# Performance work log

Measured on AMD Instinct MI355X. Metric: run time of the kernel, lower is better.

The kernel has to match this reference:

```python
import jax, jax.numpy as jnp
import numpy as np

HEADS = 16
EMBED = 1024
HEAD_DIM = EMBED // HEADS

def _split_heads(x):
    b, n, _ = x.shape
    return x.reshape(b, n, HEADS, HEAD_DIM).transpose(0, 2, 1, 3)  # b h n d

def _merge_heads(x):
    b, h, n, d = x.shape
    return x.transpose(0, 2, 1, 3).reshape(b, n, h * d)

def _attn(q_in, kv_in, Wq, bq, Wk, bk, Wv, bv, Wo, bo):
    q = _split_heads(q_in @ Wq + bq)
    k = _split_heads(kv_in @ Wk + bk)
    v = _split_heads(kv_in @ Wv + bv)
    e = jnp.einsum('bhqd,bhkd->bhqk', q, k) * (HEAD_DIM ** -0.5)
    a = jax.nn.softmax(e, axis=-1)
    o = jnp.einsum('bhqk,bhkd->bhqd', a, v)
    return _merge_heads(o) @ Wo + bo

def _layernorm(x, g, b, eps=1e-5):
    mu = jnp.mean(x, axis=-1, keepdims=True)
    var = jnp.var(x, axis=-1, keepdims=True)
    return (x - mu) * jax.lax.rsqrt(var + eps) * g + b

def setup_inputs() -> dict:
    key = jax.random.key(0)
    ks = jax.random.split(key, 20)
    s = 0.02
    d = {
        'temp_features': jax.random.normal(ks[0], (2, 2048, EMBED), jnp.float32),
        'spat_features': jax.random.normal(ks[1], (2, 2048, EMBED), jnp.float32),
    }
    names = ['t2s_Wq', 't2s_Wk', 't2s_Wv', 't2s_Wo', 's2t_Wq', 's2t_Wk', 's2t_Wv', 's2t_Wo']
    for i, nm in enumerate(names):
        d[nm] = jax.random.normal(ks[2 + i], (EMBED, EMBED), jnp.float32) * s
        d[nm.replace('W', 'b')] = jnp.zeros((EMBED,), jnp.float32)
    d['ln_g'] = jnp.ones((EMBED,), jnp.float32)
    d['ln_b'] = jnp.zeros((EMBED,), jnp.float32)
    return d

def reference(temp_features, spat_features,
              t2s_Wq, t2s_bq, t2s_Wk, t2s_bk, t2s_Wv, t2s_bv, t2s_Wo, t2s_bo,
              s2t_Wq, s2t_bq, s2t_Wk, s2t_bk, s2t_Wv, s2t_bv, s2t_Wo, s2t_bo,
              ln_g, ln_b):
    # t2s: queries from spat, keys/values from temp; residual = spat
    t2s = _attn(spat_features, temp_features, t2s_Wq, t2s_bq, t2s_Wk, t2s_bk,
                t2s_Wv, t2s_bv, t2s_Wo, t2s_bo)
    t2s_out = _layernorm(spat_features + t2s, ln_g, ln_b)
    # s2t: queries from temp, keys/values from spat; residual = temp
    s2t = _attn(temp_features, spat_features, s2t_Wq, s2t_bq, s2t_Wk, s2t_bk,
                s2t_Wv, s2t_bv, s2t_Wo, s2t_bo)
    s2t_out = _layernorm(temp_features + s2t, ln_g, ln_b)
    return (s2t_out, t2s_out)
```

## Files before the change

kernel.cpp:

```cpp
#include <hip/hip_runtime.h>
#include <stdint.h>

#define SEQ 2048
#define EMB 1024
#define NROWS 4096

typedef __bf16 bf16x8 __attribute__((ext_vector_type(8)));
typedef float f32x4 __attribute__((ext_vector_type(4)));
typedef unsigned short ushort8 __attribute__((ext_vector_type(8)));

__device__ __forceinline__ unsigned short f2bf(float f) {
  unsigned int u = __float_as_uint(f);
  u += 0x7fffu + ((u >> 16) & 1u);
  return (unsigned short)(u >> 16);
}

__device__ __forceinline__ float bf2f(unsigned short h) {
  return __uint_as_float((unsigned int)h << 16);
}

__device__ __forceinline__ f32x4 mfma16(bf16x8 a, bf16x8 b, f32x4 c) {
  return __builtin_amdgcn_mfma_f32_16x16x32_bf16(a, b, c, 0, 0, 0);
}

__device__ __forceinline__ void async_load16(const void* g, void* l) {
  auto gp = reinterpret_cast<__attribute__((address_space(1))) void*>(
      reinterpret_cast<uintptr_t>(g));
  auto lp = reinterpret_cast<__attribute__((address_space(3))) void*>(
      reinterpret_cast<uintptr_t>(l));
  __builtin_amdgcn_global_load_lds(gp, lp, 16, 0, 0);
}

__global__ __launch_bounds__(256) void prep(const float* __restrict__ t,
                                            const float* __restrict__ s,
                                            unsigned short* __restrict__ tb,
                                            unsigned short* __restrict__ sb,
                                            const float* __restrict__ W0,
                                            const float* __restrict__ W1,
                                            const float* __restrict__ W2,
                                            const float* __restrict__ W3,
                                            const float* __restrict__ W4,
                                            const float* __restrict__ W5,
                                            const float* __restrict__ W6,
                                            const float* __restrict__ W7,
                                            unsigned short* __restrict__ Wt) {
  const int bx = blockIdx.x;
  if (bx < 8192) {
    int i = bx * 256 + threadIdx.x;
    const float* x; unsigned short* y;
    if (i < NROWS * EMB / 4) { x = t; y = tb; }
    else { x = s; y = sb; i -= NROWS * EMB / 4; }
    float4 v = ((const float4*)x)[i];
    ushort4 o;
    o.x = f2bf(v.x); o.y = f2bf(v.y); o.z = f2bf(v.z); o.w = f2bf(v.w);
    ((ushort4*)y)[i] = o;
    return;
  }
  const int e = bx - 8192;
  const int z = e >> 8, tt = e & 255;
  const float* Ws[8] = {W0, W1, W2, W3, W4, W5, W6, W7};
  const float* W = Ws[z];
  unsigned short* dst = Wt + ((size_t)z << 20);
  __shared__ unsigned short tile[64][65];
  const int n0 = (tt & 15) * 64, k0 = (tt >> 4) * 64;
#pragma unroll
  for (int i = 0; i < 16; ++i) {
    const int ee = i * 256 + threadIdx.x;
    const int kk = ee >> 6, nn = ee & 63;
    tile[kk][nn] = f2bf(W[(size_t)(k0 + kk) * EMB + n0 + nn]);
  }
  __syncthreads();
#pragma unroll
  for (int i = 0; i < 16; ++i) {
    const int ee = i * 256 + threadIdx.x;
    const int nn = ee >> 6, kk = ee & 63;
    dst[(size_t)(n0 + nn) * EMB + k0 + kk] = tile[kk][nn];
  }
}

__device__ __forceinline__ void gemm_core64(const unsigned short* __restrict__ A,
                                            const unsigned short* __restrict__ Bt,
                                            int m0, int bt0,
                                            unsigned short* As, unsigned short* Bs,
                                            f32x4 (&acc)[4][4]) {
  const int tid = threadIdx.x;
  const int w = tid >> 6, lane = tid & 63;
  const int quad = lane >> 4, l16 = lane & 15;
  const int wm = w & 1, wn = w >> 1;
  const int sw8 = l16 & 7;

  const int srow = lane >> 3, p8 = lane & 7;
  const unsigned short* Ag[4];
  const unsigned short* Bg[4];
#pragma unroll
  for (int i = 0; i < 4; ++i) {
    const int r = w * 32 + i * 8 + srow;
    Ag[i] = A + (size_t)(m0 + r) * EMB + ((p8 ^ (r & 7)) * 8);
    Bg[i] = Bt + (size_t)(bt0 + r) * EMB + ((p8 ^ (r & 7)) * 8);
  }
  unsigned short* AsB[4];
  unsigned short* BsB[4];
#pragma unroll
  for (int i = 0; i < 4; ++i) {
    AsB[i] = As + (w * 32 + i * 8) * 64;
    BsB[i] = Bs + (w * 32 + i * 8) * 64;
  }

  for (int kk = 0; kk < EMB; kk += 64) {
    __syncthreads();
#pragma unroll
    for (int i = 0; i < 4; ++i) {
      async_load16(Ag[i] + kk, AsB[i]);
      async_load16(Bg[i] + kk, BsB[i]);
    }
    __syncthreads();
#pragma unroll
    for (int h = 0; h < 2; ++h) {
      bf16x8 af[4], bfr[4];
#pragma unroll
      for (int im = 0; im < 4; ++im)
        af[im] = *(const bf16x8*)(As + (wm * 64 + im * 16 + l16) * 64 +
                                  (((h * 4 + quad) ^ sw8) * 8));
#pragma unroll
      for (int in = 0; in < 4; ++in)
        bfr[in] = *(const bf16x8*)(Bs + (wn * 64 + in * 16 + l16) * 64 +
                                   (((h * 4 + quad) ^ sw8) * 8));
#pragma unroll
      for (int im = 0; im < 4; ++im)
#pragma unroll
        for (int in = 0; in < 4; ++in)
          acc[im][in] = mfma16(af[im], bfr[in], acc[im][in]);
    }
  }
}

__global__ __launch_bounds__(256, 3) void gemm_qkv(const unsigned short* __restrict__ tempb,
                                                   const unsigned short* __restrict__ spatb,
                                                   const unsigned short* __restrict__ Wt,
                                                   const float* __restrict__ bq0,
                                                   const float* __restrict__ bk0,
                                                   const float* __restrict__ bv0,
                                                   const float* __restrict__ bq1,
                                                   const float* __restrict__ bk1,
                                                   const float* __restrict__ bv1,
                                                   unsigned short* __restrict__ Qb,
                                                   unsigned short* __restrict__ Kb,
                                                   unsigned short* __restrict__ Vtb) {
  __shared__ alignas(16) unsigned short As[128 * 64];
  __shared__ alignas(16) unsigned short Bs[128 * 64];
  const int idx = blockIdx.x >> 3;
  const int dir = idx / 3, kind = idx - dir * 3;
  const int n0 = (blockIdx.x & 7) * 128;
  const unsigned short* A =
      (dir == 0) ? (kind == 0 ? tempb : spatb) : (kind == 0 ? spatb : tempb);
  const float* bias = (dir == 0) ? (kind == 0 ? bq0 : (kind == 1 ? bk0 : bv0))
                                 : (kind == 0 ? bq1 : (kind == 1 ? bk1 : bv1));

  f32x4 acc[4][4] = {};
  gemm_core64(A, Wt + ((size_t)(dir * 4 + kind) << 20), blockIdx.y * 128, n0, As, Bs, acc);

  const int tid = threadIdx.x;
  const int w = tid >> 6, lane = tid & 63;
  const int quad = lane >> 4, l16 = lane & 15;
  const int wm = w & 1, wn = w >> 1;
  const int rowb = blockIdx.y * 128 + wm * 64;
  const size_t dof = (size_t)dir * NROWS * EMB;

  if (kind == 2) {
    unsigned short* Vt = Vtb + dof;
#pragma unroll
    for (int in = 0; in < 4; ++in) {
      const int col = n0 + wn * 64 + in * 16 + l16;
      const int h = col >> 6, d = col & 63;
      const float bvv = bias[col];
#pragma unroll
      for (int im = 0; im < 4; ++im) {
        const int row = rowb + im * 16 + quad * 4;
        const int b = row >> 11, key = row & 2047;
        ushort4 o;
        o.x = f2bf(acc[im][in][0] + bvv);
        o.y = f2bf(acc[im][in][1] + bvv);
        o.z = f2bf(acc[im][in][2] + bvv);
        o.w = f2bf(acc[im][in][3] + bvv);
        *(ushort4*)(Vt + ((size_t)(b * 16 + h) * 64 + d) * SEQ + key) = o;
      }
    }
  } else {
    unsigned short* out = ((kind == 0) ? Qb : Kb) + dof;
    const float scale = (kind == 0) ? 0.18033688011112042f : 1.0f;
#pragma unroll
    for (int in = 0; in < 4; ++in) {
      const int col = n0 + wn * 64 + in * 16 + l16;
      const float bvv = bias[col];
#pragma unroll
      for (int im = 0; im < 4; ++im)
#pragma unroll
        for (int r = 0; r < 4; ++r) {
          const int row = rowb + im * 16 + quad * 4 + r;
          out[(size_t)row * EMB + col] = f2bf((acc[im][in][r] + bvv) * scale);
        }
    }
  }
}

__global__ __launch_bounds__(256, 3) void gemm_o(const unsigned short* __restrict__ Ob,
                                                 const unsigned short* __restrict__ Wt,
                                                 const float* __restrict__ bo0,
                                                 const float* __restrict__ bo1,
                                                 const float* __restrict__ temp,
                                                 const float* __restrict__ spat,
                                                 unsigned short* __restrict__ projb) {
  __shared__ alignas(16) unsigned short As[128 * 64];
  __shared__ alignas(16) unsigned short Bs[128 * 64];
  const int dir = blockIdx.x >> 3;
  const int n0 = (blockIdx.x & 7) * 128;
  const size_t dof = (size_t)dir * NROWS * EMB;
  const float* bias = dir ? bo1 : bo0;
  const float* resid = dir ? spat : temp;

  f32x4 acc[4][4] = {};
  gemm_core64(Ob + dof, Wt + ((size_t)(dir * 4 + 3) << 20), blockIdx.y * 128, n0, As, Bs,
              acc);

  const int tid = threadIdx.x;
  const int w = tid >> 6, lane = tid & 63;
  const int quad = lane >> 4, l16 = lane & 15;
  const int wm = w & 1, wn = w >> 1;
  const int rowb = blockIdx.y * 128 + wm * 64;
  unsigned short* outb = projb + dof;
#pragma unroll
  for (int in = 0; in < 4; ++in) {
    const int col = n0 + wn * 64 + in * 16 + l16;
    const float bvv = bias[col];
#pragma unroll
    for (int im = 0; im < 4; ++im)
#pragma unroll
      for (int r = 0; r < 4; ++r) {
        const int row = rowb + im * 16 + quad * 4 + r;
        const size_t off = (size_t)row * EMB + col;
        outb[off] = f2bf(acc[im][in][r] + bvv + resid[off]);
      }
  }
}

__global__ __launch_bounds__(256, 4) void flash_attn(const unsigned short* __restrict__ Qall,
                                                     const unsigned short* __restrict__ Kall,
                                                     const unsigned short* __restrict__ Vtall,
                                                     unsigned short* __restrict__ Oall) {
  __shared__ alignas(16) unsigned short Ks[64 * 64];
  __shared__ alignas(16) unsigned short Vs[64 * 64];
  __shared__ alignas(16) unsigned short Ps[4][2048];

  const int tid = threadIdx.x;
  const int w = tid >> 6, lane = tid & 63;
  const int quad = lane >> 4, l16 = lane & 15;
  const int dir = blockIdx.y >> 5, bh = blockIdx.y & 31;
  const int b = bh >> 4, h = bh & 15;
  const size_t dof = (size_t)dir * NROWS * EMB;
  const unsigned short* Q = Qall + dof;
  const unsigned short* K = Kall + dof;
  const unsigned short* Vt = Vtall + dof;
  unsigned short* O = Oall + dof;
  const int q0 = blockIdx.x * 128 + w * 32;

  bf16x8 qf[2][2];
#pragma unroll
  for (int qh = 0; qh < 2; ++qh) {
    const unsigned short* Qrow = Q + (size_t)(b * SEQ + q0 + qh * 16 + l16) * EMB + h * 64;
    qf[qh][0] = *(const bf16x8*)(Qrow + quad * 8);
    qf[qh][1] = *(const bf16x8*)(Qrow + 32 + quad * 8);
  }

  bf16x8 onesf;
#pragma unroll
  for (int i = 0; i < 8; ++i) onesf[i] = (__bf16)1.0f;

  f32x4 oaccT[2][4] = {};
  f32x4 rs[2] = {};
  unsigned short* pw = &Ps[w][0];
  const int swz = (l16 & 7) << 1;
  const int sw8 = l16 & 7;

  const int r8 = lane >> 3, p8 = lane & 7;
  const int kr0 = w * 16 + r8, kr1 = kr0 + 8;
  const unsigned short* Ksrc0 = K + (size_t)(b * SEQ + kr0) * EMB + h * 64 + ((p8 ^ (kr0 & 7)) * 8);
  const unsigned short* Ksrc1 = K + (size_t)(b * SEQ + kr1) * EMB + h * 64 + ((p8 ^ (kr1 & 7)) * 8);
  const unsigned short* Vsrc0 = Vt + ((size_t)bh * 64 + kr0) * SEQ + ((p8 ^ (kr0 & 7)) * 8);
  const unsigned short* Vsrc1 = Vt + ((size_t)bh * 64 + kr1) * SEQ + ((p8 ^ (kr1 & 7)) * 8);
  unsigned short* KsW0 = Ks + (w * 16) * 64;
  unsigned short* KsW1 = Ks + (w * 16 + 8) * 64;
  unsigned short* VsW0 = Vs + (w * 16) * 64;
  unsigned short* VsW1 = Vs + (w * 16 + 8) * 64;

  for (int kt = 0; kt < SEQ; kt += 64) {
    __syncthreads();
    async_load16(Ksrc0 + (size_t)kt * EMB, KsW0);
    async_load16(Ksrc1 + (size_t)kt * EMB, KsW1);
    async_load16(Vsrc0 + kt, VsW0);
    async_load16(Vsrc1 + kt, VsW1);
    __syncthreads();

#pragma unroll
    for (int g = 0; g < 4; ++g) {
      const int key = g * 16 + l16;
      bf16x8 kf0 = *(const bf16x8*)(Ks + key * 64 + ((quad ^ sw8) * 8));
      bf16x8 kf1 = *(const bf16x8*)(Ks + key * 64 + (((4 + quad) ^ sw8) * 8));
      const int kb = 4 * g + quad;
#pragma unroll
      for (int qh = 0; qh < 2; ++qh) {
        f32x4 z = {};
        z = mfma16(kf0, qf[qh][0], z);
        z = mfma16(kf1, qf[qh][1], z);
        uint2 pk;
        pk.x = (__float_as_uint(__builtin_amdgcn_exp2f(z[0])) >> 16) |
               (__float_as_uint(__builtin_amdgcn_exp2f(z[1])) & 0xffff0000u);
        pk.y = (__float_as_uint(__builtin_amdgcn_exp2f(z[2])) >> 16) |
               (__float_as_uint(__builtin_amdgcn_exp2f(z[3])) & 0xffff0000u);
        *(uint2*)(pw + (qh * 16 + l16) * 64 + ((kb ^ swz) << 2)) = pk;
      }
    }
    asm volatile("" ::: "memory");
    bf16x8 pb[2][2];
#pragma unroll
    for (int qh = 0; qh < 2; ++qh) {
      const int qrow = qh * 16 + l16;
      pb[qh][0] = *(const bf16x8*)(pw + qrow * 64 + (((2 * quad) ^ swz) << 2));
      pb[qh][1] = *(const bf16x8*)(pw + qrow * 64 + (((8 + 2 * quad) ^ swz) << 2));
      rs[qh] = mfma16(onesf, pb[qh][1], mfma16(onesf, pb[qh][0], rs[qh]));
    }
    asm volatile("" ::: "memory");
#pragma unroll
    for (int dg = 0; dg < 4; ++dg) {
      const int dd = dg * 16 + l16;
      bf16x8 v0 = *(const bf16x8*)(Vs + dd * 64 + ((quad ^ sw8) * 8));
      bf16x8 v1 = *(const bf16x8*)(Vs + dd * 64 + (((4 + quad) ^ sw8) * 8));
#pragma unroll
      for (int qh = 0; qh < 2; ++qh) {
        oaccT[qh][dg] = mfma16(v0, pb[qh][0], oaccT[qh][dg]);
        oaccT[qh][dg] = mfma16(v1, pb[qh][1], oaccT[qh][dg]);
      }
    }
    asm volatile("" ::: "memory");
  }

#pragma unroll
  for (int qh = 0; qh < 2; ++qh) {
    const float inv = 1.0f / rs[qh][0];
#pragma unroll
    for (int dg = 0; dg < 4; ++dg) {
      uint2 pk;
      pk.x = (unsigned int)f2bf(oaccT[qh][dg][0] * inv) |
             ((unsigned int)f2bf(oaccT[qh][dg][1] * inv) << 16);
      pk.y = (unsigned int)f2bf(oaccT[qh][dg][2] * inv) |
             ((unsigned int)f2bf(oaccT[qh][dg][3] * inv) << 16);
      const int kb = 4 * dg + quad;
      *(uint2*)(pw + l16 * 64 + ((kb ^ swz) << 2)) = pk;
    }
    asm volatile("" ::: "memory");
    const int qq = lane >> 2, cc = lane & 3;
    const int swq = (qq & 7) << 1;
    ushort8 r0 = *(const ushort8*)(pw + qq * 64 + (((4 * cc) ^ swq) << 2));
    ushort8 r1 = *(const ushort8*)(pw + qq * 64 + (((4 * cc + 2) ^ swq) << 2));
    unsigned short* Orow = O + (size_t)(b * SEQ + q0 + qh * 16 + qq) * EMB + h * 64 + cc * 16;
    *(ushort8*)(Orow) = r0;
    *(ushort8*)(Orow + 8) = r1;
    asm volatile("" ::: "memory");
  }
}

__global__ __launch_bounds__(256) void ln_k(const unsigned short* __restrict__ X,
                                            const float* __restrict__ g,
                                            const float* __restrict__ bb,
                                            float* __restrict__ out) {
  const int row = blockIdx.x;
  const int tid = threadIdx.x;
  const ushort4 hv = ((const ushort4*)(X + (size_t)row * EMB))[tid];
  float4 v;
  v.x = bf2f(hv.x); v.y = bf2f(hv.y); v.z = bf2f(hv.z); v.w = bf2f(hv.w);
  float s = v.x + v.y + v.z + v.w;
  float s2 = v.x * v.x + v.y * v.y + v.z * v.z + v.w * v.w;
#pragma unroll
  for (int o = 32; o > 0; o >>= 1) {
    s += __shfl_down(s, o);
    s2 += __shfl_down(s2, o);
  }
  __shared__ float ws[4], ws2[4];
  if ((tid & 63) == 0) { ws[tid >> 6] = s; ws2[tid >> 6] = s2; }
  __syncthreads();
  const float S = ws[0] + ws[1] + ws[2] + ws[3];
  const float S2 = ws2[0] + ws2[1] + ws2[2] + ws2[3];
  const float mu = S * (1.f / EMB);
  const float inv = rsqrtf(S2 * (1.f / EMB) - mu * mu + 1e-5f);
  const float4 gv = ((const float4*)g)[tid];
  const float4 bv = ((const float4*)bb)[tid];
  float4 o4;
  o4.x = (v.x - mu) * inv * gv.x + bv.x;
  o4.y = (v.y - mu) * inv * gv.y + bv.y;
  o4.z = (v.z - mu) * inv * gv.z + bv.z;
  o4.w = (v.w - mu) * inv * gv.w + bv.w;
  ((float4*)(out + (size_t)row * EMB))[tid] = o4;
}

extern "C" void kernel_launch(void* const* d_in, const int* in_sizes, int n_in,
                              void* d_out, int out_size, void* d_ws, size_t ws_size,
                              hipStream_t stream) {
  const float* temp = (const float*)d_in[0];
  const float* spat = (const float*)d_in[1];
  const float* lng = (const float*)d_in[18];
  const float* lnb = (const float*)d_in[19];
  float* out = (float*)d_out;

  char* base = (char*)d_ws;
  unsigned short* tempb = (unsigned short*)(base + ((size_t)0 << 20));
  unsigned short* spatb = (unsigned short*)(base + ((size_t)8 << 20));
  unsigned short* Wt = (unsigned short*)(base + ((size_t)16 << 20));
  unsigned short* Qb = (unsigned short*)(base + ((size_t)32 << 20));
  unsigned short* Kb = (unsigned short*)(base + ((size_t)48 << 20));
  unsigned short* Vtb = (unsigned short*)(base + ((size_t)64 << 20));
  unsigned short* Ob = (unsigned short*)(base + ((size_t)80 << 20));
  unsigned short* projb = (unsigned short*)(base + ((size_t)32 << 20));

  prep<<<8192 + 2048, 256, 0, stream>>>(
      temp, spat, tempb, spatb, (const float*)d_in[10], (const float*)d_in[12],
      (const float*)d_in[14], (const float*)d_in[16], (const float*)d_in[2],
      (const float*)d_in[4], (const float*)d_in[6], (const float*)d_in[8], Wt);
  gemm_qkv<<<dim3(48, 32), 256, 0, stream>>>(
      tempb, spatb, Wt, (const float*)d_in[11], (const float*)d_in[13],
      (const float*)d_in[15], (const float*)d_in[3], (const float*)d_in[5],
      (const float*)d_in[7], Qb, Kb, Vtb);
  flash_attn<<<dim3(16, 64), 256, 0, stream>>>(Qb, Kb, Vtb, Ob);
  gemm_o<<<dim3(16, 32), 256, 0, stream>>>(Ob, Wt, (const float*)d_in[17],
                                           (const float*)d_in[9], temp, spat, projb);
  ln_k<<<2 * NROWS, 256, 0, stream>>>(projb, lng, lnb, out);
}
```

Before: 312.8 us.

## Double-buffer K/V tiles in flash attention and remap blocks across XCDs

The flash attention kernel now keeps two shared-memory buffers for K and V. The next tile's async load is issued before computing on the current one, using vmcnt waits and raw barriers instead of two __syncthreads per iteration. It also remaps the block index so that blocks sharing the same (direction, batch, head) land on the same XCD, which should improve L2 reuse of K/V. Shared memory per block roughly rises by 16KB, which may lower occupancy under launch_bounds(256,4). The remap assumes a specific grid shape of 16x64.

After: 322.2 us. +3.0%, slower.

```diff
diff --git a/kernel.cpp b/kernel.cpp
--- a/kernel.cpp
+++ b/kernel.cpp
@@ -247,21 +247,25 @@
                                                      const unsigned short* __restrict__ Kall,
                                                      const unsigned short* __restrict__ Vtall,
                                                      unsigned short* __restrict__ Oall) {
-  __shared__ alignas(16) unsigned short Ks[64 * 64];
-  __shared__ alignas(16) unsigned short Vs[64 * 64];
+  __shared__ alignas(16) unsigned short Ks[2][64 * 64];
+  __shared__ alignas(16) unsigned short Vs[2][64 * 64];
   __shared__ alignas(16) unsigned short Ps[4][2048];
 
   const int tid = threadIdx.x;
   const int w = tid >> 6, lane = tid & 63;
   const int quad = lane >> 4, l16 = lane & 15;
-  const int dir = blockIdx.y >> 5, bh = blockIdx.y & 31;
+  const int phys = blockIdx.x + (blockIdx.y << 4);
+  const int xcd = phys & 7, slot = phys >> 3;
+  const int bxv = slot & 15;
+  const int byv = (xcd << 3) + (slot >> 4);
+  const int dir = byv >> 5, bh = byv & 31;
   const int b = bh >> 4, h = bh & 15;
   const size_t dof = (size_t)dir * NROWS * EMB;
   const unsigned short* Q = Qall + dof;
   const unsigned short* K = Kall + dof;
   const unsigned short* Vt = Vtall + dof;
   unsigned short* O = Oall + dof;
-  const int q0 = blockIdx.x * 128 + w * 32;
+  const int q0 = bxv * 128 + w * 32;
 
   bf16x8 qf[2][2];
 #pragma unroll
@@ -287,24 +291,39 @@
   const unsigned short* Ksrc1 = K + (size_t)(b * SEQ + kr1) * EMB + h * 64 + ((p8 ^ (kr1 & 7)) * 8);
   const unsigned short* Vsrc0 = Vt + ((size_t)bh * 64 + kr0) * SEQ + ((p8 ^ (kr0 & 7)) * 8);
   const unsigned short* Vsrc1 = Vt + ((size_t)bh * 64 + kr1) * SEQ + ((p8 ^ (kr1 & 7)) * 8);
-  unsigned short* KsW0 = Ks + (w * 16) * 64;
-  unsigned short* KsW1 = Ks + (w * 16 + 8) * 64;
-  unsigned short* VsW0 = Vs + (w * 16) * 64;
-  unsigned short* VsW1 = Vs + (w * 16 + 8) * 64;
-
+  unsigned short* KsW0 = &Ks[0][0] + (w * 16) * 64;
+  unsigned short* KsW1 = &Ks[0][0] + (w * 16 + 8) * 64;
+  unsigned short* VsW0 = &Vs[0][0] + (w * 16) * 64;
+  unsigned short* VsW1 = &Vs[0][0] + (w * 16 + 8) * 64;
+
+  async_load16(Ksrc0, KsW0);
+  async_load16(Ksrc1, KsW1);
+  async_load16(Vsrc0, VsW0);
+  async_load16(Vsrc1, VsW1);
+
+  int cur = 0;
   for (int kt = 0; kt < SEQ; kt += 64) {
-    __syncthreads();
-    async_load16(Ksrc0 + (size_t)kt * EMB, KsW0);
-    async_load16(Ksrc1 + (size_t)kt * EMB, KsW1);
-    async_load16(Vsrc0 + kt, VsW0);
-    async_load16(Vsrc1 + kt, VsW1);
-    __syncthreads();
+    const int nb = cur ^ 1;
+    if (kt + 64 < SEQ) {
+      async_load16(Ksrc0 + (size_t)(kt + 64) * EMB, KsW0 + nb * 4096);
+      async_load16(Ksrc1 + (size_t)(kt + 64) * EMB, KsW1 + nb * 4096);
+      async_load16(Vsrc0 + (kt + 64), VsW0 + nb * 4096);
+      async_load16(Vsrc1 + (kt + 64), VsW1 + nb * 4096);
+      asm volatile("s_waitcnt vmcnt(4)" ::: "memory");
+    } else {
+      asm volatile("s_waitcnt vmcnt(0)" ::: "memory");
+    }
+    __builtin_amdgcn_s_barrier();
+    asm volatile("" ::: "memory");
+
+    const unsigned short* KsC = &Ks[cur][0];
+    const unsigned short* VsC = &Vs[cur][0];
 
 #pragma unroll
     for (int g = 0; g < 4; ++g) {
       const int key = g * 16 + l16;
-      bf16x8 kf0 = *(const bf16x8*)(Ks + key * 64 + ((quad ^ sw8) * 8));
-      bf16x8 kf1 = *(const bf16x8*)(Ks + key * 64 + (((4 + quad) ^ sw8) * 8));
+      bf16x8 kf0 = *(const bf16x8*)(KsC + key * 64 + ((quad ^ sw8) * 8));
+      bf16x8 kf1 = *(const bf16x8*)(KsC + key * 64 + (((4 + quad) ^ sw8) * 8));
       const int kb = 4 * g + quad;
 #pragma unroll
       for (int qh = 0; qh < 2; ++qh) {
@@ -332,8 +351,8 @@
 #pragma unroll
     for (int dg = 0; dg < 4; ++dg) {
       const int dd = dg * 16 + l16;
-      bf16x8 v0 = *(const bf16x8*)(Vs + dd * 64 + ((quad ^ sw8) * 8));
-      bf16x8 v1 = *(const bf16x8*)(Vs + dd * 64 + (((4 + quad) ^ sw8) * 8));
+      bf16x8 v0 = *(const bf16x8*)(VsC + dd * 64 + ((quad ^ sw8) * 8));
+      bf16x8 v1 = *(const bf16x8*)(VsC + dd * 64 + (((4 + quad) ^ sw8) * 8));
 #pragma unroll
       for (int qh = 0; qh < 2; ++qh) {
         oaccT[qh][dg] = mfma16(v0, pb[qh][0], oaccT[qh][dg]);
@@ -341,6 +360,8 @@
       }
     }
     asm volatile("" ::: "memory");
+    __builtin_amdgcn_s_barrier();
+    cur ^= 1;
   }
 
 #pragma unroll
```
